# Kernel optimization log

Measured on AMD Instinct MI355X. Metric: run time of the kernel, lower is better.

Reference implementation:

```python
import jax, jax.numpy as jnp
import numpy as np
import math

HIDDEN = 1024
HEADS = 16
HEAD_DIM = HIDDEN // HEADS
B, S = 4, 2048


def setup_inputs() -> dict:
    key = jax.random.key(0)
    ks = jax.random.split(key, 9)
    std = 1.0 / math.sqrt(HIDDEN)
    return {
        "query": jax.random.normal(ks[0], (B, S, HIDDEN), jnp.float32),
        "key": jax.random.normal(ks[1], (B, S, HIDDEN), jnp.float32),
        "value": jax.random.normal(ks[2], (B, S, HIDDEN), jnp.float32),
        "q_w": jax.random.normal(ks[3], (HIDDEN, HIDDEN), jnp.float32) * std,
        "q_b": jax.random.normal(ks[4], (HIDDEN,), jnp.float32) * 0.02,
        "k_w": jax.random.normal(ks[5], (HIDDEN, HIDDEN), jnp.float32) * std,
        "k_b": jax.random.normal(ks[6], (HIDDEN,), jnp.float32) * 0.02,
        "v_w": jax.random.normal(ks[7], (HIDDEN, HIDDEN), jnp.float32) * std,
        "v_b": jax.random.normal(ks[8], (HIDDEN,), jnp.float32) * 0.02,
    }


def _split_heads(x):
    # [B, S, H] -> [B, heads, S, head_dim]
    b, s, _ = x.shape
    return x.reshape(b, s, HEADS, HEAD_DIM).transpose(0, 2, 1, 3)


def reference(query, key, value, q_w, q_b, k_w, k_b, v_w, v_b):
    # Linear projections (torch Linear: x @ W^T + b; here weights stored as [in, out])
    q = _split_heads(query @ q_w + q_b)   # [B, h, S, d]
    k = _split_heads(key @ k_w + k_b)
    v = _split_heads(value @ v_w + v_b)
    scale = 1.0 / math.sqrt(HEAD_DIM)
    scores = jnp.einsum("bhqd,bhkd->bhqk", q, k) * scale  # [B, h, S, S]
    # NOTE: faithful to source bug — context uses raw scaled scores, NOT softmax probs.
    # (softmax is computed in the original but its result is unused for the output.)
    ctx = jnp.einsum("bhqk,bhkd->bhqd", scores, v)
    ctx = ctx.transpose(0, 2, 1, 3).reshape(query.shape[0], query.shape[1], HIDDEN)
    return ctx
```

## Files before the change

### kernel.cpp

```cpp
#include <hip/hip_runtime.h>
#include <stdint.h>

#define HIDDEN 1024
#define HEADS 16
#define HEAD_DIM 64
#define BATCH 4
#define SEQ 2048
#define ROWS (BATCH * SEQ)

typedef float f32x4 __attribute__((ext_vector_type(4)));
typedef short bf16x8 __attribute__((ext_vector_type(8)));

__device__ __forceinline__ uint16_t f32_to_bf16_rne(float f) {
    uint32_t u = __float_as_uint(f);
    uint32_t r = u + 0x7FFFu + ((u >> 16) & 1u);
    return (uint16_t)(r >> 16);
}
__device__ __forceinline__ float bf16_to_f32(uint16_t u) {
    return __uint_as_float(((uint32_t)u) << 16);
}

__global__ __launch_bounds__(256) void cvt_kernel(const float* __restrict__ Xq,
                                                  const float* __restrict__ Xk,
                                                  const float* __restrict__ Xv,
                                                  uint16_t* __restrict__ Xb,
                                                  float4* __restrict__ M) {
    if (blockIdx.x < 256)
        M[blockIdx.x * 256 + threadIdx.x] = make_float4(0.f, 0.f, 0.f, 0.f);
    int z = blockIdx.x >> 12;
    const float* X = z == 0 ? Xq : (z == 1 ? Xk : Xv);
    uint16_t* out = Xb + (size_t)z * ROWS * HIDDEN;
    size_t e = ((size_t)(blockIdx.x & 4095) * 256 + threadIdx.x) * 8;
    float4 f0 = *(const float4*)(X + e);
    float4 f1 = *(const float4*)(X + e + 4);
    uint4 pk;
    pk.x = (uint32_t)f32_to_bf16_rne(f0.x) | ((uint32_t)f32_to_bf16_rne(f0.y) << 16);
    pk.y = (uint32_t)f32_to_bf16_rne(f0.z) | ((uint32_t)f32_to_bf16_rne(f0.w) << 16);
    pk.z = (uint32_t)f32_to_bf16_rne(f1.x) | ((uint32_t)f32_to_bf16_rne(f1.y) << 16);
    pk.w = (uint32_t)f32_to_bf16_rne(f1.z) | ((uint32_t)f32_to_bf16_rne(f1.w) << 16);
    *(uint4*)(out + e) = pk;
}

__global__ __launch_bounds__(256) void wt_kernel(const float* __restrict__ Wk,
                                                 const float* __restrict__ Wv,
                                                 uint16_t* __restrict__ Wt) {
    const float* W = blockIdx.z == 0 ? Wk : Wv;
    uint16_t* out = Wt + (size_t)blockIdx.z * HIDDEN * HIDDEN;
    __shared__ float tile[64][65];
    int k0 = blockIdx.x * 64, n0 = blockIdx.y * 64;
    int r = threadIdx.x >> 6, c = threadIdx.x & 63;
    for (int it = 0; it < 16; ++it) {
        int rr = r + 4 * it;
        tile[rr][c] = W[(size_t)(k0 + rr) * HIDDEN + n0 + c];
    }
    __syncthreads();
    for (int it = 0; it < 16; ++it) {
        int rr = r + 4 * it;
        out[(size_t)(n0 + rr) * HIDDEN + k0 + c] = f32_to_bf16_rne(tile[c][rr]);
    }
}

__global__ __launch_bounds__(256) void proj_gemm(const uint16_t* __restrict__ Xkv,
                                                 const uint16_t* __restrict__ Wt,
                                                 const float* __restrict__ Bk,
                                                 const float* __restrict__ Bv,
                                                 uint16_t* __restrict__ KV) {
    const int z = blockIdx.z;
    const uint16_t* X = Xkv + (size_t)z * ROWS * HIDDEN;
    const uint16_t* W = Wt + (size_t)z * HIDDEN * HIDDEN;
    const float* bias = z == 0 ? Bk : Bv;
    uint16_t* out = KV + (size_t)z * ROWS * HIDDEN;

    __shared__ uint16_t lds[16384];

    const int tid = threadIdx.x;
    const int lane = tid & 63;
    const int w = tid >> 6;
    const int wm = (w >> 1) * 64;
    const int wn = (w & 1) * 64;
    const int m_lane = lane & 15;
    const int kq = lane >> 4;
    const int m0 = blockIdx.x * 128;
    const int n0 = blockIdx.y * 128;

    f32x4 acc[4][4] = {};

    for (int kb = 0; kb < HIDDEN; kb += 64) {
        for (int t = 0; t < 4; ++t) {
            int gbase = (w * 4 + t) * 64;
            int g = gbase + lane;
            int r = g >> 3;
            int c = (g & 7) ^ (r & 7);
            const uint16_t* srcA = X + (size_t)(m0 + r) * HIDDEN + kb + c * 8;
            __builtin_amdgcn_global_load_lds(
                (const __attribute__((address_space(1))) uint32_t*)srcA,
                (__attribute__((address_space(3))) uint32_t*)(&lds[gbase * 8]),
                16, 0, 0);
            const uint16_t* srcB = W + (size_t)(n0 + r) * HIDDEN + kb + c * 8;
            __builtin_amdgcn_global_load_lds(
                (const __attribute__((address_space(1))) uint32_t*)srcB,
                (__attribute__((address_space(3))) uint32_t*)(&lds[8192 + gbase * 8]),
                16, 0, 0);
        }
        __syncthreads();
        for (int ks = 0; ks < 2; ++ks) {
            int cbase = ks * 4 + kq;
            bf16x8 af[4], bfr[4];
            for (int i = 0; i < 4; ++i) {
                int r = wm + i * 16 + m_lane;
                int p = cbase ^ (r & 7);
                af[i] = *(const bf16x8*)(&lds[r * 64 + p * 8]);
            }
            for (int j = 0; j < 4; ++j) {
                int nr = wn + j * 16 + m_lane;
                int p = cbase ^ (nr & 7);
                bfr[j] = *(const bf16x8*)(&lds[8192 + nr * 64 + p * 8]);
            }
            for (int i = 0; i < 4; ++i)
                for (int j = 0; j < 4; ++j)
                    acc[i][j] = __builtin_amdgcn_mfma_f32_16x16x32_bf16(
                        af[i], bfr[j], acc[i][j], 0, 0, 0);
        }
        __syncthreads();
    }

    for (int j = 0; j < 4; ++j) {
        int col = n0 + wn + j * 16 + m_lane;
        float bj = bias[col];
        for (int i = 0; i < 4; ++i) {
            int rbase = m0 + wm + i * 16 + kq * 4;
            for (int rg = 0; rg < 4; ++rg) {
                float v = acc[i][j][rg] + bj;
                out[(size_t)(rbase + rg) * HIDDEN + col] = f32_to_bf16_rne(v);
            }
        }
    }
}

__global__ __launch_bounds__(256) void kv_kernel(const uint16_t* __restrict__ KV,
                                                 float* __restrict__ M) {
    const uint16_t* K = KV;
    const uint16_t* V = KV + (size_t)ROWS * HIDDEN;
    const int bh = blockIdx.x;
    const int sc = blockIdx.y;
    const int b = bh >> 4, h = bh & 15;
    const int tid = threadIdx.x;
    const size_t base = ((size_t)b * SEQ + sc * 128) * HIDDEN + h * 64;

    __shared__ float kk[16][64];
    __shared__ float vv[16][64];
    float acc[4][4] = {};
    const int i0 = (tid >> 4) * 4, j0 = (tid & 15) * 4;

    for (int batch = 0; batch < 8; ++batch) {
        __syncthreads();
        {
            int t = tid & 127;
            int row = t >> 3, c = t & 7;
            const uint16_t* src =
                (tid < 128 ? K : V) + base + (size_t)(batch * 16 + row) * HIDDEN + c * 8;
            float* dst = (tid < 128 ? &kk[row][c * 8] : &vv[row][c * 8]);
            bf16x8 d = *(const bf16x8*)src;
            for (int e = 0; e < 8; ++e) dst[e] = bf16_to_f32((uint16_t)d[e]);
        }
        __syncthreads();
        for (int r = 0; r < 16; ++r) {
            f32x4 ka = *(const f32x4*)(&kk[r][i0]);
            f32x4 va = *(const f32x4*)(&vv[r][j0]);
            for (int a = 0; a < 4; ++a)
                for (int bb = 0; bb < 4; ++bb)
                    acc[a][bb] += ka[a] * va[bb];
        }
    }
    float* Mh = M + (size_t)bh * 4096;
    for (int a = 0; a < 4; ++a)
        for (int bb = 0; bb < 4; ++bb)
            atomicAdd(&Mh[(i0 + a) * 64 + j0 + bb], acc[a][bb] * 0.125f);
}

__global__ __launch_bounds__(256) void wprime_kernel(const float* __restrict__ Wq,
                                                     const float* __restrict__ bq,
                                                     const float* __restrict__ M,
                                                     uint16_t* __restrict__ Wpt,
                                                     float* __restrict__ bp) {
    const int h = blockIdx.x;
    const int r0 = blockIdx.y * 64;
    const int b = blockIdx.z;
    const int tid = threadIdx.x;

    __shared__ float Mh[64][65];
    __shared__ float Wl[64][65];
    for (int it = 0; it < 16; ++it) {
        int e = it * 256 + tid;
        int a = e >> 6, c = e & 63;
        Mh[a][c] = M[((size_t)(b * 16 + h)) * 4096 + e];
        Wl[a][c] = Wq[(size_t)(r0 + a) * HIDDEN + h * 64 + c];
    }
    __syncthreads();

    const int r = tid & 63;
    const int jbase = tid >> 6;
    float acc[16] = {};
    for (int i = 0; i < 64; ++i) {
        float wv = Wl[r][i];
        for (int jj = 0; jj < 16; ++jj)
            acc[jj] += wv * Mh[i][jbase + 4 * jj];
    }
    uint16_t* Wb = Wpt + (size_t)b * HIDDEN * HIDDEN;
    for (int jj = 0; jj < 16; ++jj) {
        int n = h * 64 + jbase + 4 * jj;
        Wb[(size_t)n * HIDDEN + r0 + r] = f32_to_bf16_rne(acc[jj]);
    }

    if (blockIdx.y == 0 && tid < 64) {
        int j = tid;
        float s = 0.f;
        for (int i = 0; i < 64; ++i) s += bq[h * 64 + i] * Mh[i][j];
        bp[b * HIDDEN + h * 64 + j] = s;
    }
}

__global__ __launch_bounds__(256) void final_gemm(const uint16_t* __restrict__ Xq,
                                                  const uint16_t* __restrict__ Wpt,
                                                  const float* __restrict__ bp,
                                                  float* __restrict__ out) {
    __shared__ uint16_t lds[16384];

    const int tid = threadIdx.x;
    const int lane = tid & 63;
    const int w = tid >> 6;
    const int wm = (w >> 1) * 64;
    const int wn = (w & 1) * 64;
    const int m_lane = lane & 15;
    const int kq = lane >> 4;
    const int m0 = blockIdx.x * 128;
    const int n0 = blockIdx.y * 128;
    const int batch = m0 >> 11;
    const uint16_t* W = Wpt + (size_t)batch * HIDDEN * HIDDEN;
    const float* bias = bp + batch * HIDDEN;

    f32x4 acc[4][4] = {};

    for (int kb = 0; kb < HIDDEN; kb += 64) {
        for (int t = 0; t < 4; ++t) {
            int gbase = (w * 4 + t) * 64;
            int g = gbase + lane;
            int r = g >> 3;
            int c = (g & 7) ^ (r & 7);
            const uint16_t* srcA = Xq + (size_t)(m0 + r) * HIDDEN + kb + c * 8;
            __builtin_amdgcn_global_load_lds(
                (const __attribute__((address_space(1))) uint32_t*)srcA,
                (__attribute__((address_space(3))) uint32_t*)(&lds[gbase * 8]),
                16, 0, 0);
            const uint16_t* srcB = W + (size_t)(n0 + r) * HIDDEN + kb + c * 8;
            __builtin_amdgcn_global_load_lds(
                (const __attribute__((address_space(1))) uint32_t*)srcB,
                (__attribute__((address_space(3))) uint32_t*)(&lds[8192 + gbase * 8]),
                16, 0, 0);
        }
        __syncthreads();
        for (int ks = 0; ks < 2; ++ks) {
            int cbase = ks * 4 + kq;
            bf16x8 af[4], bfr[4];
            for (int i = 0; i < 4; ++i) {
                int r = wm + i * 16 + m_lane;
                int p = cbase ^ (r & 7);
                af[i] = *(const bf16x8*)(&lds[r * 64 + p * 8]);
            }
            for (int j = 0; j < 4; ++j) {
                int nr = wn + j * 16 + m_lane;
                int p = cbase ^ (nr & 7);
                bfr[j] = *(const bf16x8*)(&lds[8192 + nr * 64 + p * 8]);
            }
            for (int i = 0; i < 4; ++i)
                for (int j = 0; j < 4; ++j)
                    acc[i][j] = __builtin_amdgcn_mfma_f32_16x16x32_bf16(
                        af[i], bfr[j], acc[i][j], 0, 0, 0);
        }
        __syncthreads();
    }

    for (int j = 0; j < 4; ++j) {
        int col = n0 + wn + j * 16 + m_lane;
        float bj = bias[col];
        for (int i = 0; i < 4; ++i) {
            int rbase = m0 + wm + i * 16 + kq * 4;
            for (int rg = 0; rg < 4; ++rg)
                out[(size_t)(rbase + rg) * HIDDEN + col] = acc[i][j][rg] + bj;
        }
    }
}

extern "C" void kernel_launch(void* const* d_in, const int* in_sizes, int n_in,
                              void* d_out, int out_size, void* d_ws, size_t ws_size,
                              hipStream_t stream) {
    const float* Xq = (const float*)d_in[0];
    const float* Xk = (const float*)d_in[1];
    const float* Xv = (const float*)d_in[2];
    const float* Wq = (const float*)d_in[3];
    const float* Bq = (const float*)d_in[4];
    const float* Wk = (const float*)d_in[5];
    const float* Bk = (const float*)d_in[6];
    const float* Wv = (const float*)d_in[7];
    const float* Bv = (const float*)d_in[8];
    float* out = (float*)d_out;

    char* ws = (char*)d_ws;
    uint16_t* Xb = (uint16_t*)ws;
    uint16_t* KV = (uint16_t*)(ws + 50331648);
    uint16_t* Wt = (uint16_t*)(ws + 83886080);
    float* M = (float*)(ws + 88080384);
    uint16_t* Wpt = (uint16_t*)(ws + 89128960);
    float* bp = (float*)(ws + 97517568);

    cvt_kernel<<<dim3(3 * 4096), 256, 0, stream>>>(Xq, Xk, Xv, Xb, (float4*)M);
    wt_kernel<<<dim3(16, 16, 2), 256, 0, stream>>>(Wk, Wv, Wt);

    const uint16_t* Xkv = Xb + (size_t)ROWS * HIDDEN;
    proj_gemm<<<dim3(64, 8, 2), 256, 0, stream>>>(Xkv, Wt, Bk, Bv, KV);
    kv_kernel<<<dim3(64, 16), 256, 0, stream>>>(KV, M);
    wprime_kernel<<<dim3(16, 16, 4), 256, 0, stream>>>(Wq, Bq, M, Wpt, bp);
    final_gemm<<<dim3(64, 8), 256, 0, stream>>>(Xb, Wpt, bp, out);
}
```

Baseline: 310.4 us.

## Reassociate K^T V through raw inputs to avoid projecting K and V

Instead of projecting K and V for all tokens and then forming per-head K^T V, the code now computes Xv^T Xk per batch (a 1024x1024 Gram over the sequence), multiplies by the K and V weights, and folds the bias terms in using column sums. This removes the two full projection GEMMs and the atomic-based K^T V reduction. In exchange it adds transpose kernels for Xk and Xv, two batched 1024x1024 GEMMs, and extra bf16 rounding of intermediate products, which may change accuracy.

```diff
diff --git a/kernel.cpp b/kernel.cpp
--- a/kernel.cpp
+++ b/kernel.cpp
@@ -7,6 +7,7 @@
 #define BATCH 4
 #define SEQ 2048
 #define ROWS (BATCH * SEQ)
+#define MB 1048576ull
 
 typedef float f32x4 __attribute__((ext_vector_type(4)));
 typedef short bf16x8 __attribute__((ext_vector_type(8)));
@@ -20,25 +21,42 @@
     return __uint_as_float(((uint32_t)u) << 16);
 }
 
-__global__ __launch_bounds__(256) void cvt_kernel(const float* __restrict__ Xq,
-                                                  const float* __restrict__ Xk,
-                                                  const float* __restrict__ Xv,
-                                                  uint16_t* __restrict__ Xb,
-                                                  float4* __restrict__ M) {
-    if (blockIdx.x < 256)
-        M[blockIdx.x * 256 + threadIdx.x] = make_float4(0.f, 0.f, 0.f, 0.f);
-    int z = blockIdx.x >> 12;
-    const float* X = z == 0 ? Xq : (z == 1 ? Xk : Xv);
-    uint16_t* out = Xb + (size_t)z * ROWS * HIDDEN;
-    size_t e = ((size_t)(blockIdx.x & 4095) * 256 + threadIdx.x) * 8;
-    float4 f0 = *(const float4*)(X + e);
-    float4 f1 = *(const float4*)(X + e + 4);
+__global__ __launch_bounds__(256) void cvtq_kernel(const float* __restrict__ Xq,
+                                                   uint16_t* __restrict__ Xqb) {
+    size_t e = ((size_t)blockIdx.x * 256 + threadIdx.x) * 8;
+    float4 f0 = *(const float4*)(Xq + e);
+    float4 f1 = *(const float4*)(Xq + e + 4);
     uint4 pk;
     pk.x = (uint32_t)f32_to_bf16_rne(f0.x) | ((uint32_t)f32_to_bf16_rne(f0.y) << 16);
     pk.y = (uint32_t)f32_to_bf16_rne(f0.z) | ((uint32_t)f32_to_bf16_rne(f0.w) << 16);
     pk.z = (uint32_t)f32_to_bf16_rne(f1.x) | ((uint32_t)f32_to_bf16_rne(f1.y) << 16);
     pk.w = (uint32_t)f32_to_bf16_rne(f1.z) | ((uint32_t)f32_to_bf16_rne(f1.w) << 16);
-    *(uint4*)(out + e) = pk;
+    *(uint4*)(Xqb + e) = pk;
+}
+
+__global__ __launch_bounds__(256) void cvtT_kernel(const float* __restrict__ Xk,
+                                                   const float* __restrict__ Xv,
+                                                   uint16_t* __restrict__ XkT,
+                                                   uint16_t* __restrict__ XvT) {
+    const float* X = blockIdx.z == 0 ? Xk : Xv;
+    uint16_t* XT = blockIdx.z == 0 ? XkT : XvT;
+    const int s0 = blockIdx.x * 64, p0 = blockIdx.y * 64;
+    const int tid = threadIdx.x;
+    const int w = tid >> 6, l = tid & 63;
+
+    __shared__ uint16_t tile[64 * 65];
+    for (int it = 0; it < 16; ++it) {
+        int s = it * 4 + w;
+        tile[s * 65 + l] = f32_to_bf16_rne(X[(size_t)(s0 + s) * HIDDEN + p0 + l]);
+    }
+    __syncthreads();
+    for (int pass = 0; pass < 2; ++pass) {
+        int p = (tid >> 3) + 32 * pass;
+        int c = tid & 7;
+        bf16x8 v;
+        for (int e = 0; e < 8; ++e) v[e] = (short)tile[(c * 8 + e) * 65 + p];
+        *(bf16x8*)(XT + (size_t)(p0 + p) * ROWS + s0 + c * 8) = v;
+    }
 }
 
 __global__ __launch_bounds__(256) void wt_kernel(const float* __restrict__ Wk,
@@ -60,16 +78,14 @@
     }
 }
 
-__global__ __launch_bounds__(256) void proj_gemm(const uint16_t* __restrict__ Xkv,
-                                                 const uint16_t* __restrict__ Wt,
-                                                 const float* __restrict__ Bk,
-                                                 const float* __restrict__ Bv,
-                                                 uint16_t* __restrict__ KV) {
-    const int z = blockIdx.z;
-    const uint16_t* X = Xkv + (size_t)z * ROWS * HIDDEN;
-    const uint16_t* W = Wt + (size_t)z * HIDDEN * HIDDEN;
-    const float* bias = z == 0 ? Bk : Bv;
-    uint16_t* out = KV + (size_t)z * ROWS * HIDDEN;
+__global__ __launch_bounds__(256) void gemm_bt(const uint16_t* __restrict__ A, int lda, long long aBS,
+                                               const uint16_t* __restrict__ B, int ldb, long long bBS,
+                                               uint16_t* __restrict__ C, int ldc, long long cBS,
+                                               int klen) {
+    const int bz = blockIdx.z;
+    A += (size_t)aBS * bz;
+    B += (size_t)bBS * bz;
+    C += (size_t)cBS * bz;
 
     __shared__ uint16_t lds[16384];
 
@@ -85,18 +101,18 @@
 
     f32x4 acc[4][4] = {};
 
-    for (int kb = 0; kb < HIDDEN; kb += 64) {
+    for (int kb = 0; kb < klen; kb += 64) {
         for (int t = 0; t < 4; ++t) {
             int gbase = (w * 4 + t) * 64;
             int g = gbase + lane;
             int r = g >> 3;
             int c = (g & 7) ^ (r & 7);
-            const uint16_t* srcA = X + (size_t)(m0 + r) * HIDDEN + kb + c * 8;
+            const uint16_t* srcA = A + (size_t)(m0 + r) * lda + kb + c * 8;
             __builtin_amdgcn_global_load_lds(
                 (const __attribute__((address_space(1))) uint32_t*)srcA,
                 (__attribute__((address_space(3))) uint32_t*)(&lds[gbase * 8]),
                 16, 0, 0);
-            const uint16_t* srcB = W + (size_t)(n0 + r) * HIDDEN + kb + c * 8;
+            const uint16_t* srcB = B + (size_t)(n0 + r) * ldb + kb + c * 8;
             __builtin_amdgcn_global_load_lds(
                 (const __attribute__((address_space(1))) uint32_t*)srcB,
                 (__attribute__((address_space(3))) uint32_t*)(&lds[8192 + gbase * 8]),
@@ -126,56 +142,128 @@
 
     for (int j = 0; j < 4; ++j) {
         int col = n0 + wn + j * 16 + m_lane;
-        float bj = bias[col];
         for (int i = 0; i < 4; ++i) {
             int rbase = m0 + wm + i * 16 + kq * 4;
-            for (int rg = 0; rg < 4; ++rg) {
-                float v = acc[i][j][rg] + bj;
-                out[(size_t)(rbase + rg) * HIDDEN + col] = f32_to_bf16_rne(v);
+            for (int rg = 0; rg < 4; ++rg)
+                C[(size_t)(rbase + rg) * ldc + col] = f32_to_bf16_rne(acc[i][j][rg]);
+        }
+    }
+}
+
+__global__ __launch_bounds__(256) void colsum_kernel(const uint16_t* __restrict__ XkT,
+                                                     const uint16_t* __restrict__ XvT,
+                                                     float* __restrict__ ck) {
+    const int w = threadIdx.x >> 6, l = threadIdx.x & 63;
+    const int gw = blockIdx.x * 4 + w;
+    const int z = gw >> 12;
+    const int rem = gw & 4095;
+    const int b = rem >> 10, p = rem & 1023;
+    const uint16_t* XT = z == 0 ? XkT : XvT;
+    const uint16_t* row = XT + (size_t)p * ROWS + b * SEQ;
+
+    float s = 0.f;
+    for (int it = 0; it < 4; ++it) {
+        bf16x8 v = *(const bf16x8*)(row + it * 512 + l * 8);
+        for (int e = 0; e < 8; ++e) s += bf16_to_f32((uint16_t)v[e]);
+    }
+    for (int off = 32; off; off >>= 1) s += __shfl_down(s, off);
+    if (l == 0) ck[z * 4096 + b * 1024 + p] = s;
+}
+
+__global__ __launch_bounds__(256) void uv_kernel(const uint16_t* __restrict__ Wt,
+                                                 const float* __restrict__ ck,
+                                                 float* __restrict__ uv) {
+    const int w = threadIdx.x >> 6, l = threadIdx.x & 63;
+    const int gw = blockIdx.x * 4 + w;
+    const int z = gw >> 10;
+    const int i = gw & 1023;
+    const uint16_t* wr = Wt + (size_t)z * HIDDEN * HIDDEN + (size_t)i * HIDDEN + l * 16;
+    bf16x8 w0 = *(const bf16x8*)wr;
+    bf16x8 w1 = *(const bf16x8*)(wr + 8);
+    const float* cb = ck + z * 4096;
+
+    float acc[4] = {};
+    for (int e = 0; e < 8; ++e) {
+        float we = bf16_to_f32((uint16_t)w0[e]);
+        float wf = bf16_to_f32((uint16_t)w1[e]);
+        int pa = l * 16 + e, pb = l * 16 + 8 + e;
+        for (int b = 0; b < 4; ++b)
+            acc[b] += we * cb[b * 1024 + pa] + wf * cb[b * 1024 + pb];
+    }
+    for (int b = 0; b < 4; ++b)
+        for (int off = 32; off; off >>= 1) acc[b] += __shfl_down(acc[b], off);
+    if (l == 0)
+        for (int b = 0; b < 4; ++b) uv[z * 4096 + b * 1024 + i] = acc[b];
+}
+
+__global__ __launch_bounds__(256) void mfold_kernel(const uint16_t* __restrict__ T,
+                                                    const uint16_t* __restrict__ Wt,
+                                                    const float* __restrict__ Bk,
+                                                    const float* __restrict__ Bv,
+                                                    const float* __restrict__ uv,
+                                                    float* __restrict__ M) {
+    const int b = blockIdx.x >> 4, h = blockIdx.x & 15;
+    const uint16_t* A = T + (size_t)b * MB + (size_t)h * 64 * HIDDEN;
+    const uint16_t* B = Wt + (size_t)HIDDEN * HIDDEN + (size_t)h * 64 * HIDDEN;
+
+    __shared__ uint16_t lds[8192];
+
+    const int tid = threadIdx.x;
+    const int lane = tid & 63;
+    const int w = tid >> 6;
+    const int m_lane = lane & 15;
+    const int kq = lane >> 4;
+
+    f32x4 acc[4] = {};
+
+    for (int kb = 0; kb < HIDDEN; kb += 64) {
+        for (int t = 0; t < 2; ++t) {
+            int gbase = (w * 2 + t) * 64;
+            int g = gbase + lane;
+            int r = g >> 3;
+            int c = (g & 7) ^ (r & 7);
+            const uint16_t* srcA = A + (size_t)r * HIDDEN + kb + c * 8;
+            __builtin_amdgcn_global_load_lds(
+                (const __attribute__((address_space(1))) uint32_t*)srcA,
+                (__attribute__((address_space(3))) uint32_t*)(&lds[gbase * 8]),
+                16, 0, 0);
+            const uint16_t* srcB = B + (size_t)r * HIDDEN + kb + c * 8;
+            __builtin_amdgcn_global_load_lds(
+                (const __attribute__((address_space(1))) uint32_t*)srcB,
+                (__attribute__((address_space(3))) uint32_t*)(&lds[4096 + gbase * 8]),
+                16, 0, 0);
+        }
+        __syncthreads();
+        for (int ks = 0; ks < 2; ++ks) {
+            int cbase = ks * 4 + kq;
+            int r = w * 16 + m_lane;
+            int p = cbase ^ (r & 7);
+            bf16x8 af = *(const bf16x8*)(&lds[r * 64 + p * 8]);
+            for (int j = 0; j < 4; ++j) {
+                int nr = j * 16 + m_lane;
+                int pb = cbase ^ (nr & 7);
+                bf16x8 bfr = *(const bf16x8*)(&lds[4096 + nr * 64 + pb * 8]);
+                acc[j] = __builtin_amdgcn_mfma_f32_16x16x32_bf16(af, bfr, acc[j], 0, 0, 0);
             }
         }
-    }
-}
-
-__global__ __launch_bounds__(256) void kv_kernel(const uint16_t* __restrict__ KV,
-                                                 float* __restrict__ M) {
-    const uint16_t* K = KV;
-    const uint16_t* V = KV + (size_t)ROWS * HIDDEN;
-    const int bh = blockIdx.x;
-    const int sc = blockIdx.y;
-    const int b = bh >> 4, h = bh & 15;
-    const int tid = threadIdx.x;
-    const size_t base = ((size_t)b * SEQ + sc * 128) * HIDDEN + h * 64;
-
-    __shared__ float kk[16][64];
-    __shared__ float vv[16][64];
-    float acc[4][4] = {};
-    const int i0 = (tid >> 4) * 4, j0 = (tid & 15) * 4;
-
-    for (int batch = 0; batch < 8; ++batch) {
-        __syncthreads();
-        {
-            int t = tid & 127;
-            int row = t >> 3, c = t & 7;
-            const uint16_t* src =
-                (tid < 128 ? K : V) + base + (size_t)(batch * 16 + row) * HIDDEN + c * 8;
-            float* dst = (tid < 128 ? &kk[row][c * 8] : &vv[row][c * 8]);
-            bf16x8 d = *(const bf16x8*)src;
-            for (int e = 0; e < 8; ++e) dst[e] = bf16_to_f32((uint16_t)d[e]);
-        }
-        __syncthreads();
-        for (int r = 0; r < 16; ++r) {
-            f32x4 ka = *(const f32x4*)(&kk[r][i0]);
-            f32x4 va = *(const f32x4*)(&vv[r][j0]);
-            for (int a = 0; a < 4; ++a)
-                for (int bb = 0; bb < 4; ++bb)
-                    acc[a][bb] += ka[a] * va[bb];
-        }
-    }
-    float* Mh = M + (size_t)bh * 4096;
-    for (int a = 0; a < 4; ++a)
-        for (int bb = 0; bb < 4; ++bb)
-            atomicAdd(&Mh[(i0 + a) * 64 + j0 + bb], acc[a][bb] * 0.125f);
+        __syncthreads();
+    }
+
+    const float* u_ = uv + b * 1024;
+    const float* v_ = uv + 4096 + b * 1024;
+    float* Mout = M + ((size_t)(b * 16 + h)) * 4096;
+    for (int j = 0; j < 4; ++j) {
+        int col = j * 16 + m_lane;
+        int gj = h * 64 + col;
+        float bvj = Bv[gj];
+        float vj = v_[gj] + 2048.f * bvj;
+        for (int rg = 0; rg < 4; ++rg) {
+            int i = w * 16 + kq * 4 + rg;
+            int gi = h * 64 + i;
+            float val = 0.125f * (acc[j][rg] + u_[gi] * bvj + Bk[gi] * vj);
+            Mout[i * 64 + col] = val;
+        }
+    }
 }
 
 __global__ __launch_bounds__(256) void wprime_kernel(const float* __restrict__ Wq,
@@ -306,19 +394,30 @@
     float* out = (float*)d_out;
 
     char* ws = (char*)d_ws;
-    uint16_t* Xb = (uint16_t*)ws;
-    uint16_t* KV = (uint16_t*)(ws + 50331648);
-    uint16_t* Wt = (uint16_t*)(ws + 83886080);
-    float* M = (float*)(ws + 88080384);
-    uint16_t* Wpt = (uint16_t*)(ws + 89128960);
-    float* bp = (float*)(ws + 97517568);
-
-    cvt_kernel<<<dim3(3 * 4096), 256, 0, stream>>>(Xq, Xk, Xv, Xb, (float4*)M);
+    uint16_t* Xqb = (uint16_t*)(ws);
+    uint16_t* XvT = (uint16_t*)(ws + 16 * MB);
+    uint16_t* XkT = (uint16_t*)(ws + 32 * MB);
+    uint16_t* Wt  = (uint16_t*)(ws + 48 * MB);
+    uint16_t* H   = (uint16_t*)(ws + 52 * MB);
+    float*    M   = (float*)   (ws + 60 * MB);
+    float*    ck  = (float*)   (ws + 61 * MB);
+    float*    uvb = (float*)   (ws + 61 * MB + 32768);
+    float*    bp  = (float*)   (ws + 61 * MB + 65536);
+    uint16_t* T   = XvT;
+    uint16_t* Wpt = XkT;
+
+    cvtq_kernel<<<dim3(4096), 256, 0, stream>>>(Xq, Xqb);
+    cvtT_kernel<<<dim3(128, 16, 2), 256, 0, stream>>>(Xk, Xv, XkT, XvT);
     wt_kernel<<<dim3(16, 16, 2), 256, 0, stream>>>(Wk, Wv, Wt);
 
-    const uint16_t* Xkv = Xb + (size_t)ROWS * HIDDEN;
-    proj_gemm<<<dim3(64, 8, 2), 256, 0, stream>>>(Xkv, Wt, Bk, Bv, KV);
-    kv_kernel<<<dim3(64, 16), 256, 0, stream>>>(KV, M);
+    gemm_bt<<<dim3(8, 8, 4), 256, 0, stream>>>(XvT, ROWS, 2048ll, XkT, ROWS, 2048ll,
+                                               H, HIDDEN, (long long)(MB / 1), 2048);
+    colsum_kernel<<<dim3(2048), 256, 0, stream>>>(XkT, XvT, ck);
+    uv_kernel<<<dim3(512), 256, 0, stream>>>(Wt, ck, uvb);
+
+    gemm_bt<<<dim3(8, 8, 4), 256, 0, stream>>>(Wt, HIDDEN, 0ll, H, HIDDEN, (long long)MB,
+                                               T, HIDDEN, (long long)MB, 1024);
+    mfold_kernel<<<dim3(64), 256, 0, stream>>>(T, Wt, Bk, Bv, uvb, M);
     wprime_kernel<<<dim3(16, 16, 4), 256, 0, stream>>>(Wq, Bq, M, Wpt, bp);
-    final_gemm<<<dim3(64, 8), 256, 0, stream>>>(Xb, Wpt, bp, out);
-}
+    final_gemm<<<dim3(64, 8), 256, 0, stream>>>(Xqb, Wpt, bp, out);
+}
```

Result: faster. 299.4 us (-3.6%).
